# Performance work log

Measured on AMD Instinct MI355X. Metric: run time of the kernel, lower is better.

## Reference

```python
import jax, jax.numpy as jnp
import numpy as np
from jax import lax

B, C, H, W = 8, 512, 16, 16
Di, N, R, K = 1024, 16, 32, 4  # d_inner, d_state, dt_rank, num scan directions
EPS = 1e-5


def _ln(x, g, b):
    mu = x.mean(-1, keepdims=True)
    var = ((x - mu) ** 2).mean(-1, keepdims=True)
    return (x - mu) * lax.rsqrt(var + EPS) * g + b


def _ss2d_core(xc, x_proj_w, dt_w, dt_b, A_logs, Ds):
    # xc: (b, Di, H, W) after depthwise conv + SiLU. 4-direction selective scan.
    b = xc.shape[0]
    L = H * W
    x_flat = xc.reshape(b, Di, L)
    x_wh = xc.transpose(0, 1, 3, 2).reshape(b, Di, L)
    x_hwwh = jnp.stack([x_flat, x_wh], 1)                  # (b,2,Di,L)
    xs = jnp.concatenate([x_hwwh, x_hwwh[..., ::-1]], 1)   # (b,K,Di,L)
    x_dbl = jnp.einsum('bkdl,kcd->bkcl', xs, x_proj_w)     # (b,K,R+2N,L)
    dts, Bs, Cs = x_dbl[:, :, :R], x_dbl[:, :, R:R + N], x_dbl[:, :, R + N:]
    dts = jnp.einsum('bkrl,kdr->bkdl', dts, dt_w)
    delta = jax.nn.softplus(dts + dt_b[None, :, :, None])  # (b,K,Di,L)
    A = -jnp.exp(A_logs).reshape(K, Di, N)                 # (K,Di,N)

    def step(h, inp):
        d, u, Bl, Cl = inp  # d,u:(b,K,Di)  Bl,Cl:(b,K,N)
        h = jnp.exp(d[..., None] * A) * h + (d * u)[..., None] * Bl[:, :, None, :]
        yl = jnp.einsum('bkdn,bkn->bkd', h, Cl)
        return h, yl

    inps = (delta.transpose(3, 0, 1, 2), xs.transpose(3, 0, 1, 2),
            Bs.transpose(3, 0, 1, 2), Cs.transpose(3, 0, 1, 2))
    h0 = jnp.zeros((b, K, Di, N), xc.dtype)
    _, ys = lax.scan(step, h0, inps)                       # (L,b,K,Di)
    ys = ys.transpose(1, 2, 3, 0) + xs * Ds.reshape(1, K, Di, 1)  # + D*u skip
    inv = ys[:, 2:4, :, ::-1]
    wh = ys[:, 1].reshape(b, Di, W, H).transpose(0, 1, 3, 2).reshape(b, Di, L)
    invwh = inv[:, 1].reshape(b, Di, W, H).transpose(0, 1, 3, 2).reshape(b, Di, L)
    y = ys[:, 0] + inv[:, 0] + wh + invwh                  # (b,Di,L)
    return y.transpose(0, 2, 1).reshape(b, H, W, Di)


def _conv_ffn(x, ffn_conv_w, bn_g, bn_b, bn_mean, bn_var, fc1_w, fc2_w):
    x = lax.conv_general_dilated(x, ffn_conv_w, (1, 1), [(1, 1), (1, 1)],
                                 dimension_numbers=('NCHW', 'OIHW', 'NCHW'))
    x = ((x - bn_mean[:, None, None]) * lax.rsqrt(bn_var + EPS)[:, None, None]
         * bn_g[:, None, None] + bn_b[:, None, None])
    x = jnp.clip(x, 0.0, 6.0)                              # ReLU6
    x = jnp.einsum('bchw,oc->bohw', x, fc1_w)              # 1x1 conv fc1
    x = jax.nn.gelu(x, approximate=False)
    return jnp.einsum('bchw,oc->bohw', x, fc2_w)           # 1x1 conv fc2


def _forward(x, y, ln1_g, ln1_b, in_proj_w, conv_w, conv_b, x_proj_w, dt_w,
             dt_b, A_logs, Ds, out_norm_g, out_norm_b, out_proj_w, ffn_conv_w,
             bn_g, bn_b, bn_mean, bn_var, fc1_w, fc2_w, lin1_w, lin1_b,
             lin2_w, lin2_b):
    # --- VSSBlock: LN -> SS2D -> residual ---
    x1 = x.transpose(0, 2, 3, 1)                           # (B,H,W,C)
    xn = _ln(x1, ln1_g, ln1_b)
    xz = jnp.einsum('bhwc,oc->bhwo', xn, in_proj_w)        # in_proj (no bias)
    xa, z = xz[..., :Di], xz[..., Di:]
    xc = xa.transpose(0, 3, 1, 2)                          # (B,Di,H,W)
    xc = lax.conv_general_dilated(xc, conv_w, (1, 1), [(1, 1), (1, 1)],
                                  feature_group_count=Di,
                                  dimension_numbers=('NCHW', 'OIHW', 'NCHW'))
    xc = jax.nn.silu(xc + conv_b[:, None, None])
    yc = _ss2d_core(xc, x_proj_w, dt_w, dt_b, A_logs, Ds)  # (B,H,W,Di)
    yc = _ln(yc, out_norm_g, out_norm_b) * jax.nn.silu(z)
    vss = x1 + jnp.einsum('bhwd,od->bhwo', yc, out_proj_w)
    # --- ConvFFN ---
    xm = _conv_ffn(vss.transpose(0, 3, 1, 2), ffn_conv_w, bn_g, bn_b, bn_mean,
                   bn_var, fc1_w, fc2_w)                   # (B,C,H,W)
    # --- channel attention: both pools are AdaptiveAvgPool2d(1), so max==avg ---
    pooled = y.mean(axis=(2, 3))                           # (B,C)
    lin = jax.nn.relu(pooled @ lin1_w.T + lin1_b) @ lin2_w.T + lin2_b
    gate = jax.nn.sigmoid(2.0 * lin)                       # linear_max + linear_avg
    return gate[:, :, None, None] * xm


def setup_inputs() -> dict:
    key = jax.random.key(0)
    ks = jax.random.split(key, 16)
    n = lambda i, shape, s=0.05: jax.random.normal(ks[i], shape, jnp.float32) * s
    return {
        'x': n(0, (B, C, H, W), 1.0),
        'y': n(1, (B, C, H, W), 1.0),
        'ln1_g': jnp.ones((C,), jnp.float32), 'ln1_b': jnp.zeros((C,), jnp.float32),
        'in_proj_w': n(2, (2 * Di, C)),
        'conv_w': n(3, (Di, 1, 3, 3), 0.2), 'conv_b': jnp.zeros((Di,), jnp.float32),
        'x_proj_w': n(4, (K, R + 2 * N, Di)),
        'dt_w': n(5, (K, Di, R), 0.1), 'dt_b': n(6, (K, Di), 0.1),
        'A_logs': n(7, (K * Di, N), 0.1), 'Ds': jnp.ones((K * Di,), jnp.float32),
        'out_norm_g': jnp.ones((Di,), jnp.float32), 'out_norm_b': jnp.zeros((Di,), jnp.float32),
        'out_proj_w': n(8, (C, Di)),
        'ffn_conv_w': n(9, (C, C, 3, 3)),
        'bn_g': jnp.ones((C,), jnp.float32), 'bn_b': jnp.zeros((C,), jnp.float32),
        'bn_mean': jnp.zeros((C,), jnp.float32), 'bn_var': jnp.ones((C,), jnp.float32),
        'fc1_w': n(10, (C, C)), 'fc2_w': n(11, (C, C)),
        'lin1_w': n(12, (C // 2, C)), 'lin1_b': jnp.zeros((C // 2,), jnp.float32),
        'lin2_w': n(13, (C, C // 2)), 'lin2_b': jnp.zeros((C,), jnp.float32),
    }


def reference(x, y, ln1_g, ln1_b, in_proj_w, conv_w, conv_b, x_proj_w, dt_w,
              dt_b, A_logs, Ds, out_norm_g, out_norm_b, out_proj_w, ffn_conv_w,
              bn_g, bn_b, bn_mean, bn_var, fc1_w, fc2_w, lin1_w, lin1_b,
              lin2_w, lin2_b):
    return _forward(x, y, ln1_g, ln1_b, in_proj_w, conv_w, conv_b, x_proj_w,
                    dt_w, dt_b, A_logs, Ds, out_norm_g, out_norm_b, out_proj_w,
                    ffn_conv_w, bn_g, bn_b, bn_mean, bn_var, fc1_w, fc2_w,
                    lin1_w, lin1_b, lin2_w, lin2_b)
```

## Files before the change

kernel.cpp:

```cpp
#include <hip/hip_runtime.h>
#include <hip/hip_bf16.h>
#include <math.h>

#define DEV_INLINE __device__ __forceinline__

constexpr int B_ = 8, C_ = 512, L_ = 256;
constexpr float EPS_ = 1e-5f;

typedef __attribute__((ext_vector_type(8))) short bf16x8;
typedef __attribute__((ext_vector_type(4))) float f32x4;

DEV_INLINE int lmap1(int l) { return ((l & 15) << 4) | (l >> 4); }
DEV_INLINE float sigmoidf_(float x) { return 1.f / (1.f + __expf(-x)); }
DEV_INLINE float siluf_(float x) { return x * sigmoidf_(x); }
DEV_INLINE float ex2_(float x) { return __builtin_amdgcn_exp2f(x); }

DEV_INLINE unsigned pk2(float a, float b) {
    __hip_bfloat16 x = __float2bfloat16(a), y = __float2bfloat16(b);
    unsigned short ux = *reinterpret_cast<unsigned short*>(&x);
    unsigned short uy = *reinterpret_cast<unsigned short*>(&y);
    return ((unsigned)uy << 16) | ux;
}

__global__ __launch_bounds__(256) void k_pool(const float* __restrict__ y, float* __restrict__ pooled) {
    int bc = blockIdx.x;
    int t = threadIdx.x;
    __shared__ float red[256];
    red[t] = y[bc * 256 + t];
    __syncthreads();
    for (int s = 128; s > 0; s >>= 1) { if (t < s) red[t] += red[t + s]; __syncthreads(); }
    if (t == 0) pooled[bc] = red[0] * (1.f / 256.f);
}

__global__ __launch_bounds__(256) void k_gate(const float* __restrict__ pooled,
                                              const float* __restrict__ lin1_w, const float* __restrict__ lin1_b,
                                              const float* __restrict__ lin2_w, const float* __restrict__ lin2_b,
                                              float* __restrict__ gate) {
    int b = blockIdx.x;
    int t = threadIdx.x;
    __shared__ float p[512];
    __shared__ float h1[256];
    p[t] = pooled[b * 512 + t];
    p[t + 256] = pooled[b * 512 + t + 256];
    __syncthreads();
    float s = lin1_b[t];
    const float4* wp1 = (const float4*)(lin1_w + t * 512);
    #pragma unroll 4
    for (int c = 0; c < 128; ++c) {
        float4 pv = *(const float4*)(p + c * 4);
        float4 wv = wp1[c];
        s = fmaf(pv.x, wv.x, s); s = fmaf(pv.y, wv.y, s);
        s = fmaf(pv.z, wv.z, s); s = fmaf(pv.w, wv.w, s);
    }
    h1[t] = fmaxf(s, 0.f);
    __syncthreads();
    #pragma unroll
    for (int cc = 0; cc < 2; ++cc) {
        int c = t + cc * 256;
        float s2 = lin2_b[c];
        const float4* wp2 = (const float4*)(lin2_w + c * 256);
        #pragma unroll 4
        for (int j = 0; j < 64; ++j) {
            float4 hv = *(const float4*)(h1 + j * 4);
            float4 wv = wp2[j];
            s2 = fmaf(hv.x, wv.x, s2); s2 = fmaf(hv.y, wv.y, s2);
            s2 = fmaf(hv.z, wv.z, s2); s2 = fmaf(hv.w, wv.w, s2);
        }
        gate[b * 512 + c] = sigmoidf_(2.f * s2);
    }
}

__global__ __launch_bounds__(256) void k_ln(const float* __restrict__ x, const float* __restrict__ g,
                                            const float* __restrict__ bta, float* __restrict__ xn) {
    int pos = blockIdx.x;
    int b = pos >> 8, l = pos & 255;
    int t = threadIdx.x;
    float v0 = x[(b * C_ + t) * L_ + l];
    float v1 = x[(b * C_ + t + 256) * L_ + l];
    __shared__ float red[256];
    red[t] = v0 + v1;
    __syncthreads();
    for (int s = 128; s > 0; s >>= 1) { if (t < s) red[t] += red[t + s]; __syncthreads(); }
    float mu = red[0] * (1.f / 512.f);
    __syncthreads();
    float d0 = v0 - mu, d1 = v1 - mu;
    red[t] = d0 * d0 + d1 * d1;
    __syncthreads();
    for (int s = 128; s > 0; s >>= 1) { if (t < s) red[t] += red[t + s]; __syncthreads(); }
    float rs = rsqrtf(red[0] * (1.f / 512.f) + EPS_);
    xn[pos * C_ + t] = d0 * rs * g[t] + bta[t];
    xn[pos * C_ + t + 256] = d1 * rs * g[t + 256] + bta[t + 256];
}

__global__ __launch_bounds__(256) void k_wcast5(const float* __restrict__ ip, const float* __restrict__ xp,
                                                const float* __restrict__ op, const float* __restrict__ f1,
                                                const float* __restrict__ f2, const float* __restrict__ dtw,
                                                __hip_bfloat16* __restrict__ dst) {
    size_t e = ((size_t)blockIdx.x * 256 + threadIdx.x) * 4;
    const float* src; size_t off;
    if (e < 1048576) { src = ip; off = e; }
    else if (e < 1310720) { src = xp; off = e - 1048576; }
    else if (e < 1835008) { src = op; off = e - 1310720; }
    else if (e < 2097152) { src = f1; off = e - 1835008; }
    else if (e < 2359296) { src = f2; off = e - 2097152; }
    else { src = dtw; off = e - 2359296; }
    float4 v = *(const float4*)(src + off);
    uint2 o; o.x = pk2(v.x, v.y); o.y = pk2(v.z, v.w);
    *(uint2*)(dst + e) = o;
}

__global__ __launch_bounds__(256) void k_wcast(const float* __restrict__ w, __hip_bfloat16* __restrict__ wt) {
    int gid = blockIdx.x * 256 + threadIdx.x;
    const float* src = w + (size_t)gid * 9;
    #pragma unroll
    for (int tap = 0; tap < 9; ++tap) wt[(size_t)tap * 262144 + gid] = __float2bfloat16(src[tap]);
}

enum { M_INPROJ = 0, M_XDBL = 1, M_OUTPROJ = 2, M_FC1 = 3, M_FC2 = 4, M_DELTA = 5 };

template <int MODE>
__global__ __launch_bounds__(256) void gemm_mfma(const float* __restrict__ Af, const __hip_bfloat16* __restrict__ Wb,
                                                 float* __restrict__ O, float* __restrict__ O2,
                                                 const float* __restrict__ AUX, __hip_bfloat16* __restrict__ Ob) {
    constexpr int KK = (MODE == M_XDBL || MODE == M_OUTPROJ) ? 1024 : (MODE == M_DELTA) ? 32 : 512;
    __shared__ short Asm[64 * 32];
    __shared__ short Bsm[64 * 32];
    const int t = threadIdx.x;
    const int lane = t & 63, wv = t >> 6;
    int m0, n0 = 0, kdir = 0, bq = 0;
    if constexpr (MODE == M_XDBL) { m0 = blockIdx.x * 64; kdir = blockIdx.y; }
    else if constexpr (MODE == M_FC2) { bq = blockIdx.x >> 3; m0 = (blockIdx.x & 7) * 64; n0 = blockIdx.y * 64; }
    else { m0 = blockIdx.x * 64; n0 = blockIdx.y * 64; }
    const int kdel = (m0 >> 8) & 3;

    const int r_ = t >> 2, kq = t & 3;
    const int skey = (r_ >> 1) & 3;
    uint4* adst = (uint4*)(Asm + r_ * 32) + (kq ^ skey);
    uint4* bdst = (uint4*)(Bsm + r_ * 32) + (kq ^ skey);

    const float* arowf = nullptr;
    const __hip_bfloat16* arowb = nullptr;
    if constexpr (MODE == M_INPROJ) arowf = Af + (size_t)(m0 + r_) * 512 + kq * 8;
    else if constexpr (MODE == M_XDBL) {
        int m = m0 + r_; int b = m >> 8, l = m & 255;
        int lm = (kdir < 2) ? l : 255 - l;
        arowf = Af + (size_t)((b * 2 + (kdir & 1)) * 256 + lm) * 1024 + kq * 8;
    } else if constexpr (MODE == M_OUTPROJ) arowf = Af + (size_t)(m0 + r_) * 1024 + kq * 8;
    else if constexpr (MODE == M_FC1) arowf = Af + (size_t)(m0 + r_) * 512 + kq * 8;
    else if constexpr (MODE == M_DELTA) arowf = Af + (size_t)(m0 + r_) * 64 + kq * 8;
    else arowb = Wb + (size_t)(m0 + r_) * 512 + kq * 8;

    const __hip_bfloat16* browb = nullptr;
    const float* browf = nullptr;
    if constexpr (MODE == M_INPROJ) browb = Wb + (size_t)(n0 + r_) * 512 + kq * 8;
    else if constexpr (MODE == M_XDBL) browb = Wb + (size_t)(kdir * 64 + r_) * 1024 + kq * 8;
    else if constexpr (MODE == M_OUTPROJ) browb = Wb + (size_t)(n0 + r_) * 1024 + kq * 8;
    else if constexpr (MODE == M_FC1) browb = Wb + (size_t)(n0 + r_) * 512 + kq * 8;
    else if constexpr (MODE == M_DELTA) browb = Wb + ((size_t)(kdel * 1024 + n0 + r_)) * 32 + kq * 8;
    else browf = Af + (size_t)(bq * 256 + n0 + r_) * 512 + kq * 8;

    f32x4 acc[4];
    #pragma unroll
    for (int nf = 0; nf < 4; ++nf) acc[nf] = (f32x4){0.f, 0.f, 0.f, 0.f};

    for (int k0 = 0; k0 < KK; k0 += 32) {
        __syncthreads();
        if constexpr (MODE == M_FC2) {
            *adst = *(const uint4*)(arowb + k0);
            float4 u0 = *(const float4*)(browf + k0);
            float4 u1 = *(const float4*)(browf + k0 + 4);
            uint4 pk; pk.x = pk2(u0.x, u0.y); pk.y = pk2(u0.z, u0.w); pk.z = pk2(u1.x, u1.y); pk.w = pk2(u1.z, u1.w);
            *bdst = pk;
        } else {
            float4 u0 = *(const float4*)(arowf + k0);
            float4 u1 = *(const float4*)(arowf + k0 + 4);
            uint4 pk; pk.x = pk2(u0.x, u0.y); pk.y = pk2(u0.z, u0.w); pk.z = pk2(u1.x, u1.y); pk.w = pk2(u1.z, u1.w);
            *adst = pk;
            *bdst = *(const uint4*)(browb + k0);
        }
        __syncthreads();
        int mrow = wv * 16 + (lane & 15);
        int ks = lane >> 4;
        bf16x8 af = *(const bf16x8*)(Asm + mrow * 32 + ((ks ^ ((mrow >> 1) & 3)) * 8));
        #pragma unroll
        for (int nf = 0; nf < 4; ++nf) {
            int nrow = nf * 16 + (lane & 15);
            bf16x8 bfv = *(const bf16x8*)(Bsm + nrow * 32 + ((ks ^ ((nrow >> 1) & 3)) * 8));
            acc[nf] = __builtin_amdgcn_mfma_f32_16x16x32_bf16(af, bfv, acc[nf], 0, 0, 0);
        }
    }

    const int mlb = (lane >> 4) * 4, nl = lane & 15;
    #pragma unroll
    for (int nf = 0; nf < 4; ++nf) {
        #pragma unroll
        for (int j = 0; j < 4; ++j) {
            float v = acc[nf][j];
            int m_loc = wv * 16 + mlb + j;
            int n_loc = nf * 16 + nl;
            if constexpr (MODE == M_INPROJ) {
                int m = m0 + m_loc, n = n0 + n_loc;
                if (n0 < 1024) O[(size_t)m * 1024 + n] = v;
                else O2[(size_t)m * 1024 + (n - 1024)] = v;
            } else if constexpr (MODE == M_XDBL) {
                int m = m0 + m_loc; int b = m >> 8, l = m & 255;
                O[((size_t)(b * 4 + kdir) * 256 + l) * 64 + n_loc] = v;
            } else if constexpr (MODE == M_OUTPROJ) {
                int m = m0 + m_loc, n = n0 + n_loc; int b = m >> 8, l = m & 255;
                float f = AUX[((size_t)b * 512 + n) * 256 + l] + v;
                Ob[(size_t)m * 512 + n] = __float2bfloat16(f);
            } else if constexpr (MODE == M_FC1) {
                int m = m0 + m_loc, n = n0 + n_loc;
                O[(size_t)m * 512 + n] = 0.5f * v * (1.f + erff(v * 0.70710678118f));
            } else if constexpr (MODE == M_DELTA) {
                int m = m0 + m_loc, n = n0 + n_loc;
                int bkk = m >> 8, l = m & 255;
                float v2 = v + AUX[kdel * 1024 + n];
                float dlt = (v2 > 20.f) ? v2 : __logf(1.f + __expf(v2));
                O[((((size_t)bkk * 32) + (n >> 5)) * 256 + l) * 32 + (n & 31)] = dlt;
            } else {
                int c = m0 + m_loc, n = n0 + n_loc;
                O[((size_t)(bq * 512 + c)) * 256 + n] = v * AUX[bq * 512 + c];
            }
        }
    }
}

__global__ __launch_bounds__(256) void k_dwconv2(const float* __restrict__ xa, const float* __restrict__ cw,
                                                 const float* __restrict__ cb, float* __restrict__ xs_t) {
    int pos = blockIdx.x;
    int b = pos >> 8, l = pos & 255;
    int h = l >> 4, w = l & 15;
    int t = threadIdx.x;
    int d = t * 4;
    float wv[36];
    {
        const float4* cp = (const float4*)(cw + (size_t)d * 9);
        #pragma unroll
        for (int j = 0; j < 9; ++j) { float4 v = cp[j]; wv[j*4] = v.x; wv[j*4+1] = v.y; wv[j*4+2] = v.z; wv[j*4+3] = v.w; }
    }
    float4 bias = *(const float4*)(cb + d);
    float a0 = bias.x, a1 = bias.y, a2 = bias.z, a3 = bias.w;
    #pragma unroll
    for (int ky = -1; ky <= 1; ++ky) {
        int hh = h + ky;
        if ((unsigned)hh >= 16u) continue;
        #pragma unroll
        for (int kx = -1; kx <= 1; ++kx) {
            int ww = w + kx;
            if ((unsigned)ww >= 16u) continue;
            float4 v = *(const float4*)(xa + (size_t)(b * 256 + hh * 16 + ww) * 1024 + d);
            int tap = (ky + 1) * 3 + (kx + 1);
            a0 = fmaf(v.x, wv[0 * 9 + tap], a0);
            a1 = fmaf(v.y, wv[1 * 9 + tap], a1);
            a2 = fmaf(v.z, wv[2 * 9 + tap], a2);
            a3 = fmaf(v.w, wv[3 * 9 + tap], a3);
        }
    }
    float4 o; o.x = siluf_(a0); o.y = siluf_(a1); o.z = siluf_(a2); o.w = siluf_(a3);
    *(float4*)(xs_t + ((size_t)(b * 2 + 0) * 256 + l) * 1024 + d) = o;
    *(float4*)(xs_t + ((size_t)(b * 2 + 1) * 256 + lmap1(l)) * 1024 + d) = o;
}

__global__ __launch_bounds__(512) void k_scan7(const float* __restrict__ xs_t, const float* __restrict__ x_dbl,
                                               const float* __restrict__ A_logs, const float* __restrict__ Ds,
                                               float* __restrict__ dys) {
    const int bk = blockIdx.x >> 5;
    const int db = blockIdx.x & 31;
    const int b = bk >> 2, k = bk & 3;
    const int t = threadIdx.x;
    const int c = t >> 5, dd = t & 31;
    const int d = db * 32 + dd;
    const bool rev = (k >= 2);

    __shared__ float Ssh[16][33];
    __shared__ float locH[16][32][17];

    float An2[16];
    {
        const float* alp = A_logs + (size_t)(k * 1024 + d) * 16;
        #pragma unroll
        for (int i = 0; i < 16; ++i) An2[i] = -__expf(alp[i]) * 1.44269504088896f;
    }
    const float Dv = Ds[k * 1024 + d];

    const int lbeg = c * 16;
    float* yp = dys + (((size_t)bk * 32 + db) * 256 + lbeg) * 32 + dd;
    const float* up = xs_t + ((size_t)(b * 2 + (k & 1)) * 256 + (rev ? 255 - lbeg : lbeg)) * 1024 + d;
    const ptrdiff_t ustr = rev ? -1024 : 1024;
    const float* xc = x_dbl + (size_t)bk * 256 * 64 + lbeg * 64;

    float h[16];
    #pragma unroll
    for (int i = 0; i < 16; ++i) h[i] = 0.f;
    float S = 0.f;

    #pragma unroll 4
    for (int li = 0; li < 16; ++li) {
        float dl = yp[li * 32];
        float u = up[(ptrdiff_t)li * ustr];
        S += dl;
        float du = dl * u;
        #pragma unroll
        for (int q = 0; q < 4; ++q) {
            float4 Bq = *(const float4*)(xc + li * 64 + 32 + q * 4);
            h[q*4+0] = fmaf(ex2_(dl * An2[q*4+0]), h[q*4+0], du * Bq.x);
            h[q*4+1] = fmaf(ex2_(dl * An2[q*4+1]), h[q*4+1], du * Bq.y);
            h[q*4+2] = fmaf(ex2_(dl * An2[q*4+2]), h[q*4+2], du * Bq.z);
            h[q*4+3] = fmaf(ex2_(dl * An2[q*4+3]), h[q*4+3], du * Bq.w);
        }
    }
    Ssh[c][dd] = S;
    #pragma unroll
    for (int i = 0; i < 16; ++i) locH[c][dd][i] = h[i];
    __syncthreads();

    #pragma unroll
    for (int i = 0; i < 16; ++i) h[i] = 0.f;
    for (int j = 0; j < c; ++j) {
        float Sj = Ssh[j][dd];
        #pragma unroll
        for (int i = 0; i < 16; ++i) h[i] = fmaf(ex2_(Sj * An2[i]), h[i], locH[j][dd][i]);
    }

    #pragma unroll 4
    for (int li = 0; li < 16; ++li) {
        float dl = yp[li * 32];
        float u = up[(ptrdiff_t)li * ustr];
        float du = dl * u;
        float yv = 0.f;
        #pragma unroll
        for (int q = 0; q < 4; ++q) {
            float4 Bq = *(const float4*)(xc + li * 64 + 32 + q * 4);
            float4 Cq = *(const float4*)(xc + li * 64 + 48 + q * 4);
            h[q*4+0] = fmaf(ex2_(dl * An2[q*4+0]), h[q*4+0], du * Bq.x); yv = fmaf(h[q*4+0], Cq.x, yv);
            h[q*4+1] = fmaf(ex2_(dl * An2[q*4+1]), h[q*4+1], du * Bq.y); yv = fmaf(h[q*4+1], Cq.y, yv);
            h[q*4+2] = fmaf(ex2_(dl * An2[q*4+2]), h[q*4+2], du * Bq.z); yv = fmaf(h[q*4+2], Cq.z, yv);
            h[q*4+3] = fmaf(ex2_(dl * An2[q*4+3]), h[q*4+3], du * Bq.w); yv = fmaf(h[q*4+3], Cq.w, yv);
        }
        yp[li * 32] = yv + u * Dv;
    }
}

__global__ __launch_bounds__(256) void k_combine(const float* __restrict__ dys, const float* __restrict__ z,
                                                 const float* __restrict__ g, const float* __restrict__ bb,
                                                 float* __restrict__ yc) {
    int pos = blockIdx.x;
    int b = pos >> 8, l = pos & 255;
    int t = threadIdx.x;
    int lw = lmap1(l);
    int db0 = t >> 5, dd = t & 31;
    float v[4];
    float psum = 0.f;
    #pragma unroll
    for (int q = 0; q < 4; ++q) {
        int dbq = db0 + q * 8;
        float s0 = dys[((((size_t)(b * 4 + 0) * 32) + dbq) * 256 + l) * 32 + dd];
        float s1 = dys[((((size_t)(b * 4 + 1) * 32) + dbq) * 256 + lw) * 32 + dd];
        float s2 = dys[((((size_t)(b * 4 + 2) * 32) + dbq) * 256 + (255 - l)) * 32 + dd];
        float s3 = dys[((((size_t)(b * 4 + 3) * 32) + dbq) * 256 + (255 - lw)) * 32 + dd];
        v[q] = s0 + s1 + s2 + s3;
        psum += v[q];
    }
    __shared__ float red[256];
    red[t] = psum;
    __syncthreads();
    for (int s = 128; s > 0; s >>= 1) { if (t < s) red[t] += red[t + s]; __syncthreads(); }
    float mu = red[0] * (1.f / 1024.f);
    __syncthreads();
    float p2 = 0.f;
    #pragma unroll
    for (int q = 0; q < 4; ++q) { float ddv = v[q] - mu; p2 += ddv * ddv; }
    red[t] = p2;
    __syncthreads();
    for (int s = 128; s > 0; s >>= 1) { if (t < s) red[t] += red[t + s]; __syncthreads(); }
    float rs = rsqrtf(red[0] * (1.f / 1024.f) + EPS_);
    #pragma unroll
    for (int q = 0; q < 4; ++q) {
        int d = (db0 + q * 8) * 32 + dd;
        float zn = z[(size_t)pos * 1024 + d];
        yc[(size_t)pos * 1024 + d] = ((v[q] - mu) * rs * g[d] + bb[d]) * siluf_(zn);
    }
}

__global__ __launch_bounds__(256) void k_conv2m(const __hip_bfloat16* __restrict__ vssb,
                                                const __hip_bfloat16* __restrict__ wt,
                                                float* __restrict__ convp) {
    __shared__ short Asm[18 * 18 * 32];
    __shared__ short Bsm[9 * 64 * 32];
    const int b = blockIdx.x, co0 = blockIdx.y * 64, split = blockIdx.z;
    const int t = threadIdx.x;
    const int lane = t & 63, wid = t >> 6;
    const int wcol = lane & 15, slot = lane >> 4;

    f32x4 acc[4][4];
    #pragma unroll
    for (int r = 0; r < 4; ++r)
        #pragma unroll
        for (int g = 0; g < 4; ++g) acc[r][g] = (f32x4){0.f, 0.f, 0.f, 0.f};

    for (int ch = 0; ch < 2; ++ch) {
        const int ci0 = split * 64 + ch * 32;
        __syncthreads();
        for (int i = t; i < 324; i += 256) {
            int row = i / 18, col = i - row * 18;
            uint4 v0 = {0,0,0,0}, v1 = {0,0,0,0}, v2 = {0,0,0,0}, v3 = {0,0,0,0};
            if (row >= 1 && row <= 16 && col >= 1 && col <= 16) {
                const uint4* src = (const uint4*)(vssb + ((size_t)(b * 256 + (row - 1) * 16 + (col - 1)) * 512 + ci0));
                v0 = src[0]; v1 = src[1]; v2 = src[2]; v3 = src[3];
            }
            uint4* dst = (uint4*)(Asm + i * 32);
            int key = (col >> 1) & 3;
            dst[0 ^ key] = v0; dst[1 ^ key] = v1; dst[2 ^ key] = v2; dst[3 ^ key] = v3;
        }
        for (int i = t; i < 576; i += 256) {
            int tap = i >> 6, col = i & 63;
            const uint4* src = (const uint4*)(wt + ((size_t)(tap * 512 + co0 + col) * 512 + ci0));
            uint4* dst = (uint4*)(Bsm + i * 32);
            int key = (col >> 1) & 3;
            dst[0 ^ key] = src[0]; dst[1 ^ key] = src[1]; dst[2 ^ key] = src[2]; dst[3 ^ key] = src[3];
        }
        __syncthreads();
        #pragma unroll
        for (int tap = 0; tap < 9; ++tap) {
            const int ky = tap / 3, kx = tap - ky * 3;
            bf16x8 af[4], bfr[4];
            #pragma unroll
            for (int r = 0; r < 4; ++r) {
                int crow = wid * 4 + r + ky;
                int ccol = wcol + kx;
                int s2 = slot ^ ((ccol >> 1) & 3);
                af[r] = *(const bf16x8*)(Asm + ((crow * 18 + ccol) * 32 + s2 * 8));
            }
            #pragma unroll
            for (int g = 0; g < 4; ++g) {
                int col = g * 16 + wcol;
                int s2 = slot ^ ((col >> 1) & 3);
                bfr[g] = *(const bf16x8*)(Bsm + ((tap * 64 + col) * 32 + s2 * 8));
            }
            #pragma unroll
            for (int r = 0; r < 4; ++r)
                #pragma unroll
                for (int g = 0; g < 4; ++g)
                    acc[r][g] = __builtin_amdgcn_mfma_f32_16x16x32_bf16(af[r], bfr[g], acc[r][g], 0, 0, 0);
        }
    }
    float* base = convp + (size_t)split * 1048576 + (size_t)b * 512 * 256;
    #pragma unroll
    for (int r = 0; r < 4; ++r) {
        int h = wid * 4 + r;
        #pragma unroll
        for (int g = 0; g < 4; ++g) {
            int co = co0 + g * 16 + wcol;
            *(f32x4*)(base + (size_t)co * 256 + h * 16 + slot * 4) = acc[r][g];
        }
    }
}

__global__ __launch_bounds__(256) void k_convred2(const float* __restrict__ convp,
                                                  const float* __restrict__ bn_g, const float* __restrict__ bn_b,
                                                  const float* __restrict__ bn_mean, const float* __restrict__ bn_var,
                                                  float* __restrict__ t1) {
    int b = blockIdx.x >> 7, cb = (blockIdx.x >> 3) & 15, pb = blockIdx.x & 7;
    int co0 = cb * 32, pos0 = pb * 32;
    int t = threadIdx.x;
    int ti = t >> 5, tj = t & 31;
    __shared__ float tile[32][33];
    #pragma unroll
    for (int r = 0; r < 4; ++r) {
        int co = co0 + ti + r * 8;
        size_t idx = ((size_t)b * 512 + co) * 256 + pos0 + tj;
        float s = 0.f;
        #pragma unroll
        for (int sp = 0; sp < 8; ++sp) s += convp[idx + (size_t)sp * 1048576];
        float o = (s - bn_mean[co]) * rsqrtf(bn_var[co] + EPS_) * bn_g[co] + bn_b[co];
        tile[ti + r * 8][tj] = fminf(fmaxf(o, 0.f), 6.f);
    }
    __syncthreads();
    #pragma unroll
    for (int r = 0; r < 4; ++r) {
        int pos = pos0 + ti + r * 8;
        t1[((size_t)b * 256 + pos) * 512 + co0 + tj] = tile[tj][ti + r * 8];
    }
}

extern "C" void kernel_launch(void* const* d_in, const int* in_sizes, int n_in,
                              void* d_out, int out_size, void* d_ws, size_t ws_size,
                              hipStream_t stream) {
    const float* x = (const float*)d_in[0];
    const float* y = (const float*)d_in[1];
    const float* ln1_g = (const float*)d_in[2];
    const float* ln1_b = (const float*)d_in[3];
    const float* in_proj_w = (const float*)d_in[4];
    const float* conv_w = (const float*)d_in[5];
    const float* conv_b = (const float*)d_in[6];
    const float* x_proj_w = (const float*)d_in[7];
    const float* dt_w = (const float*)d_in[8];
    const float* dt_b = (const float*)d_in[9];
    const float* A_logs = (const float*)d_in[10];
    const float* Ds = (const float*)d_in[11];
    const float* out_norm_g = (const float*)d_in[12];
    const float* out_norm_b = (const float*)d_in[13];
    const float* out_proj_w = (const float*)d_in[14];
    const float* ffn_conv_w = (const float*)d_in[15];
    const float* bn_g = (const float*)d_in[16];
    const float* bn_b = (const float*)d_in[17];
    const float* bn_mean = (const float*)d_in[18];
    const float* bn_var = (const float*)d_in[19];
    const float* fc1_w = (const float*)d_in[20];
    const float* fc2_w = (const float*)d_in[21];
    const float* lin1_w = (const float*)d_in[22];
    const float* lin1_b = (const float*)d_in[23];
    const float* lin2_w = (const float*)d_in[24];
    const float* lin2_b = (const float*)d_in[25];
    float* out = (float*)d_out;

    char* ws = (char*)d_ws;
    size_t off = 0;
    auto alloc = [&](size_t nf) { float* p = (float*)(ws + off); off += nf * sizeof(float); return p; };
    float* xn    = alloc(2048u * 512);
    float* xa    = alloc(2048u * 1024);
    float* z     = alloc(2048u * 1024);
    float* xs_t  = alloc(2u * 2048 * 1024);
    float* x_dbl = alloc(8u * 4 * 256 * 64);
    float* ys_t  = alloc(4u * 2048 * 1024);
    float* wb    = alloc(1245184);
    float* pooled = alloc(4096);
    float* gate   = alloc(4096);

    float* yc = xa;
    float* t1 = xs_t;
    float* t2 = xs_t + 2048u * 512;
    __hip_bfloat16* vssb = (__hip_bfloat16*)xn;
    __hip_bfloat16* w_t  = (__hip_bfloat16*)z;
    float* convp = ys_t;
    __hip_bfloat16* inprojb = (__hip_bfloat16*)wb;
    __hip_bfloat16* xprojb  = inprojb + 1048576;
    __hip_bfloat16* outprojb = xprojb + 262144;
    __hip_bfloat16* fc1b = outprojb + 524288;
    __hip_bfloat16* fc2b = fc1b + 262144;
    __hip_bfloat16* dtwb = fc2b + 262144;

    k_wcast5<<<2432, 256, 0, stream>>>(in_proj_w, x_proj_w, out_proj_w, fc1_w, fc2_w, dt_w, inprojb);
    k_pool<<<4096, 256, 0, stream>>>(y, pooled);
    k_gate<<<8, 256, 0, stream>>>(pooled, lin1_w, lin1_b, lin2_w, lin2_b, gate);
    k_ln<<<2048, 256, 0, stream>>>(x, ln1_g, ln1_b, xn);
    gemm_mfma<M_INPROJ><<<dim3(32, 32), 256, 0, stream>>>(xn, inprojb, xa, z, nullptr, nullptr);
    k_dwconv2<<<2048, 256, 0, stream>>>(xa, conv_w, conv_b, xs_t);
    gemm_mfma<M_XDBL><<<dim3(32, 4), 256, 0, stream>>>(xs_t, xprojb, x_dbl, nullptr, nullptr, nullptr);
    gemm_mfma<M_DELTA><<<dim3(128, 16), 256, 0, stream>>>(x_dbl, dtwb, ys_t, nullptr, dt_b, nullptr);
    k_scan7<<<1024, 512, 0, stream>>>(xs_t, x_dbl, A_logs, Ds, ys_t);
    k_combine<<<2048, 256, 0, stream>>>(ys_t, z, out_norm_g, out_norm_b, yc);
    k_wcast<<<1024, 256, 0, stream>>>(ffn_conv_w, w_t);
    gemm_mfma<M_OUTPROJ><<<dim3(32, 8), 256, 0, stream>>>(yc, outprojb, nullptr, nullptr, x, vssb);
    k_conv2m<<<dim3(8, 8, 8), 256, 0, stream>>>(vssb, w_t, convp);
    k_convred2<<<1024, 256, 0, stream>>>(convp, bn_g, bn_b, bn_mean, bn_var, t1);
    gemm_mfma<M_FC1><<<dim3(32, 8), 256, 0, stream>>>(t1, fc1b, t2, nullptr, nullptr, nullptr);
    gemm_mfma<M_FC2><<<dim3(64, 4), 256, 0, stream>>>(t2, fc2b, out, nullptr, gate, nullptr);
}
```

Baseline: 259.7 us.

## Emit bf16 activations from producer kernels and merge conv weight cast

Producer kernels (layernorm, combine, conv reduction, FC1 GELU epilogue) now write bf16 instead of fp32. The consuming GEMMs can then copy A tiles straight into shared memory without converting, which halves activation traffic and drops the per-tile packing. The separate conv-weight cast kernel is merged into the batch weight-cast launch, removing one launch. The scan kernel also keeps delta and u in registers from its first pass instead of reloading them in the second, at the cost of more register pressure.

```diff
diff --git a/kernel.cpp b/kernel.cpp
--- a/kernel.cpp
+++ b/kernel.cpp
@@ -71,7 +71,7 @@
 }
 
 __global__ __launch_bounds__(256) void k_ln(const float* __restrict__ x, const float* __restrict__ g,
-                                            const float* __restrict__ bta, float* __restrict__ xn) {
+                                            const float* __restrict__ bta, __hip_bfloat16* __restrict__ xnb) {
     int pos = blockIdx.x;
     int b = pos >> 8, l = pos & 255;
     int t = threadIdx.x;
@@ -88,41 +88,43 @@
     __syncthreads();
     for (int s = 128; s > 0; s >>= 1) { if (t < s) red[t] += red[t + s]; __syncthreads(); }
     float rs = rsqrtf(red[0] * (1.f / 512.f) + EPS_);
-    xn[pos * C_ + t] = d0 * rs * g[t] + bta[t];
-    xn[pos * C_ + t + 256] = d1 * rs * g[t + 256] + bta[t + 256];
-}
-
-__global__ __launch_bounds__(256) void k_wcast5(const float* __restrict__ ip, const float* __restrict__ xp,
+    xnb[pos * C_ + t] = __float2bfloat16(d0 * rs * g[t] + bta[t]);
+    xnb[pos * C_ + t + 256] = __float2bfloat16(d1 * rs * g[t + 256] + bta[t + 256]);
+}
+
+__global__ __launch_bounds__(256) void k_wcast6(const float* __restrict__ ip, const float* __restrict__ xp,
                                                 const float* __restrict__ op, const float* __restrict__ f1,
                                                 const float* __restrict__ f2, const float* __restrict__ dtw,
-                                                __hip_bfloat16* __restrict__ dst) {
-    size_t e = ((size_t)blockIdx.x * 256 + threadIdx.x) * 4;
-    const float* src; size_t off;
-    if (e < 1048576) { src = ip; off = e; }
-    else if (e < 1310720) { src = xp; off = e - 1048576; }
-    else if (e < 1835008) { src = op; off = e - 1310720; }
-    else if (e < 2097152) { src = f1; off = e - 1835008; }
-    else if (e < 2359296) { src = f2; off = e - 2097152; }
-    else { src = dtw; off = e - 2359296; }
-    float4 v = *(const float4*)(src + off);
-    uint2 o; o.x = pk2(v.x, v.y); o.y = pk2(v.z, v.w);
-    *(uint2*)(dst + e) = o;
-}
-
-__global__ __launch_bounds__(256) void k_wcast(const float* __restrict__ w, __hip_bfloat16* __restrict__ wt) {
-    int gid = blockIdx.x * 256 + threadIdx.x;
-    const float* src = w + (size_t)gid * 9;
-    #pragma unroll
-    for (int tap = 0; tap < 9; ++tap) wt[(size_t)tap * 262144 + gid] = __float2bfloat16(src[tap]);
+                                                const float* __restrict__ fw, __hip_bfloat16* __restrict__ dst) {
+    if (blockIdx.x < 2432) {
+        size_t e = ((size_t)blockIdx.x * 256 + threadIdx.x) * 4;
+        const float* src; size_t off;
+        if (e < 1048576) { src = ip; off = e; }
+        else if (e < 1310720) { src = xp; off = e - 1048576; }
+        else if (e < 1835008) { src = op; off = e - 1310720; }
+        else if (e < 2097152) { src = f1; off = e - 1835008; }
+        else if (e < 2359296) { src = f2; off = e - 2097152; }
+        else { src = dtw; off = e - 2359296; }
+        float4 v = *(const float4*)(src + off);
+        uint2 o; o.x = pk2(v.x, v.y); o.y = pk2(v.z, v.w);
+        *(uint2*)(dst + e) = o;
+    } else {
+        int gid = (blockIdx.x - 2432) * 256 + threadIdx.x;
+        __hip_bfloat16* wt = dst + 2490368;
+        const float* src = fw + (size_t)gid * 9;
+        #pragma unroll
+        for (int tap = 0; tap < 9; ++tap) wt[(size_t)tap * 262144 + gid] = __float2bfloat16(src[tap]);
+    }
 }
 
 enum { M_INPROJ = 0, M_XDBL = 1, M_OUTPROJ = 2, M_FC1 = 3, M_FC2 = 4, M_DELTA = 5 };
 
 template <int MODE>
-__global__ __launch_bounds__(256) void gemm_mfma(const float* __restrict__ Af, const __hip_bfloat16* __restrict__ Wb,
+__global__ __launch_bounds__(256) void gemm_mfma(const void* __restrict__ Aptr, const __hip_bfloat16* __restrict__ Wb,
                                                  float* __restrict__ O, float* __restrict__ O2,
                                                  const float* __restrict__ AUX, __hip_bfloat16* __restrict__ Ob) {
     constexpr int KK = (MODE == M_XDBL || MODE == M_OUTPROJ) ? 1024 : (MODE == M_DELTA) ? 32 : 512;
+    constexpr bool A_COPY = (MODE == M_INPROJ || MODE == M_OUTPROJ || MODE == M_FC1 || MODE == M_FC2);
     __shared__ short Asm[64 * 32];
     __shared__ short Bsm[64 * 32];
     const int t = threadIdx.x;
@@ -140,24 +142,23 @@
 
     const float* arowf = nullptr;
     const __hip_bfloat16* arowb = nullptr;
-    if constexpr (MODE == M_INPROJ) arowf = Af + (size_t)(m0 + r_) * 512 + kq * 8;
+    if constexpr (MODE == M_INPROJ) arowb = (const __hip_bfloat16*)Aptr + (size_t)(m0 + r_) * 512 + kq * 8;
     else if constexpr (MODE == M_XDBL) {
         int m = m0 + r_; int b = m >> 8, l = m & 255;
         int lm = (kdir < 2) ? l : 255 - l;
-        arowf = Af + (size_t)((b * 2 + (kdir & 1)) * 256 + lm) * 1024 + kq * 8;
-    } else if constexpr (MODE == M_OUTPROJ) arowf = Af + (size_t)(m0 + r_) * 1024 + kq * 8;
-    else if constexpr (MODE == M_FC1) arowf = Af + (size_t)(m0 + r_) * 512 + kq * 8;
-    else if constexpr (MODE == M_DELTA) arowf = Af + (size_t)(m0 + r_) * 64 + kq * 8;
+        arowf = (const float*)Aptr + (size_t)((b * 2 + (kdir & 1)) * 256 + lm) * 1024 + kq * 8;
+    } else if constexpr (MODE == M_OUTPROJ) arowb = (const __hip_bfloat16*)Aptr + (size_t)(m0 + r_) * 1024 + kq * 8;
+    else if constexpr (MODE == M_FC1) arowb = (const __hip_bfloat16*)Aptr + (size_t)(m0 + r_) * 512 + kq * 8;
+    else if constexpr (MODE == M_DELTA) arowf = (const float*)Aptr + (size_t)(m0 + r_) * 64 + kq * 8;
     else arowb = Wb + (size_t)(m0 + r_) * 512 + kq * 8;
 
     const __hip_bfloat16* browb = nullptr;
-    const float* browf = nullptr;
     if constexpr (MODE == M_INPROJ) browb = Wb + (size_t)(n0 + r_) * 512 + kq * 8;
     else if constexpr (MODE == M_XDBL) browb = Wb + (size_t)(kdir * 64 + r_) * 1024 + kq * 8;
     else if constexpr (MODE == M_OUTPROJ) browb = Wb + (size_t)(n0 + r_) * 1024 + kq * 8;
     else if constexpr (MODE == M_FC1) browb = Wb + (size_t)(n0 + r_) * 512 + kq * 8;
     else if constexpr (MODE == M_DELTA) browb = Wb + ((size_t)(kdel * 1024 + n0 + r_)) * 32 + kq * 8;
-    else browf = Af + (size_t)(bq * 256 + n0 + r_) * 512 + kq * 8;
+    else browb = (const __hip_bfloat16*)Aptr + (size_t)(bq * 256 + n0 + r_) * 512 + kq * 8;
 
     f32x4 acc[4];
     #pragma unroll
@@ -165,19 +166,15 @@
 
     for (int k0 = 0; k0 < KK; k0 += 32) {
         __syncthreads();
-        if constexpr (MODE == M_FC2) {
+        if constexpr (A_COPY) {
             *adst = *(const uint4*)(arowb + k0);
-            float4 u0 = *(const float4*)(browf + k0);
-            float4 u1 = *(const float4*)(browf + k0 + 4);
-            uint4 pk; pk.x = pk2(u0.x, u0.y); pk.y = pk2(u0.z, u0.w); pk.z = pk2(u1.x, u1.y); pk.w = pk2(u1.z, u1.w);
-            *bdst = pk;
         } else {
             float4 u0 = *(const float4*)(arowf + k0);
             float4 u1 = *(const float4*)(arowf + k0 + 4);
             uint4 pk; pk.x = pk2(u0.x, u0.y); pk.y = pk2(u0.z, u0.w); pk.z = pk2(u1.x, u1.y); pk.w = pk2(u1.z, u1.w);
             *adst = pk;
-            *bdst = *(const uint4*)(browb + k0);
-        }
+        }
+        *bdst = *(const uint4*)(browb + k0);
         __syncthreads();
         int mrow = wv * 16 + (lane & 15);
         int ks = lane >> 4;
@@ -211,7 +208,8 @@
                 Ob[(size_t)m * 512 + n] = __float2bfloat16(f);
             } else if constexpr (MODE == M_FC1) {
                 int m = m0 + m_loc, n = n0 + n_loc;
-                O[(size_t)m * 512 + n] = 0.5f * v * (1.f + erff(v * 0.70710678118f));
+                float gl = 0.5f * v * (1.f + erff(v * 0.70710678118f));
+                Ob[(size_t)m * 512 + n] = __float2bfloat16(gl);
             } else if constexpr (MODE == M_DELTA) {
                 int m = m0 + m_loc, n = n0 + n_loc;
                 int bkk = m >> 8, l = m & 255;
@@ -262,7 +260,7 @@
     *(float4*)(xs_t + ((size_t)(b * 2 + 1) * 256 + lmap1(l)) * 1024 + d) = o;
 }
 
-__global__ __launch_bounds__(512) void k_scan7(const float* __restrict__ xs_t, const float* __restrict__ x_dbl,
+__global__ __launch_bounds__(512) void k_scan8(const float* __restrict__ xs_t, const float* __restrict__ x_dbl,
                                                const float* __restrict__ A_logs, const float* __restrict__ Ds,
                                                float* __restrict__ dys) {
     const int bk = blockIdx.x >> 5;
@@ -294,11 +292,13 @@
     #pragma unroll
     for (int i = 0; i < 16; ++i) h[i] = 0.f;
     float S = 0.f;
-
-    #pragma unroll 4
+    float dls[16], us_[16];
+
+    #pragma unroll
     for (int li = 0; li < 16; ++li) {
         float dl = yp[li * 32];
         float u = up[(ptrdiff_t)li * ustr];
+        dls[li] = dl; us_[li] = u;
         S += dl;
         float du = dl * u;
         #pragma unroll
@@ -323,10 +323,10 @@
         for (int i = 0; i < 16; ++i) h[i] = fmaf(ex2_(Sj * An2[i]), h[i], locH[j][dd][i]);
     }
 
-    #pragma unroll 4
+    #pragma unroll
     for (int li = 0; li < 16; ++li) {
-        float dl = yp[li * 32];
-        float u = up[(ptrdiff_t)li * ustr];
+        float dl = dls[li];
+        float u = us_[li];
         float du = dl * u;
         float yv = 0.f;
         #pragma unroll
@@ -344,7 +344,7 @@
 
 __global__ __launch_bounds__(256) void k_combine(const float* __restrict__ dys, const float* __restrict__ z,
                                                  const float* __restrict__ g, const float* __restrict__ bb,
-                                                 float* __restrict__ yc) {
+                                                 __hip_bfloat16* __restrict__ ycb) {
     int pos = blockIdx.x;
     int b = pos >> 8, l = pos & 255;
     int t = threadIdx.x;
@@ -379,7 +379,8 @@
     for (int q = 0; q < 4; ++q) {
         int d = (db0 + q * 8) * 32 + dd;
         float zn = z[(size_t)pos * 1024 + d];
-        yc[(size_t)pos * 1024 + d] = ((v[q] - mu) * rs * g[d] + bb[d]) * siluf_(zn);
+        float o = ((v[q] - mu) * rs * g[d] + bb[d]) * siluf_(zn);
+        ycb[(size_t)pos * 1024 + d] = __float2bfloat16(o);
     }
 }
 
@@ -460,7 +461,7 @@
 __global__ __launch_bounds__(256) void k_convred2(const float* __restrict__ convp,
                                                   const float* __restrict__ bn_g, const float* __restrict__ bn_b,
                                                   const float* __restrict__ bn_mean, const float* __restrict__ bn_var,
-                                                  float* __restrict__ t1) {
+                                                  __hip_bfloat16* __restrict__ t1b) {
     int b = blockIdx.x >> 7, cb = (blockIdx.x >> 3) & 15, pb = blockIdx.x & 7;
     int co0 = cb * 32, pos0 = pb * 32;
     int t = threadIdx.x;
@@ -480,7 +481,7 @@
     #pragma unroll
     for (int r = 0; r < 4; ++r) {
         int pos = pos0 + ti + r * 8;
-        t1[((size_t)b * 256 + pos) * 512 + co0 + tj] = tile[tj][ti + r * 8];
+        t1b[((size_t)b * 256 + pos) * 512 + co0 + tj] = __float2bfloat16(tile[tj][ti + r * 8]);
     }
 }
 
@@ -524,15 +525,15 @@
     float* xs_t  = alloc(2u * 2048 * 1024);
     float* x_dbl = alloc(8u * 4 * 256 * 64);
     float* ys_t  = alloc(4u * 2048 * 1024);
-    float* wb    = alloc(1245184);
+    float* wb    = alloc(2424832);
     float* pooled = alloc(4096);
     float* gate   = alloc(4096);
 
-    float* yc = xa;
-    float* t1 = xs_t;
-    float* t2 = xs_t + 2048u * 512;
+    __hip_bfloat16* xnb = (__hip_bfloat16*)xn;
     __hip_bfloat16* vssb = (__hip_bfloat16*)xn;
-    __hip_bfloat16* w_t  = (__hip_bfloat16*)z;
+    __hip_bfloat16* ycb = (__hip_bfloat16*)xa;
+    __hip_bfloat16* t1b = (__hip_bfloat16*)xs_t;
+    __hip_bfloat16* t2b = (__hip_bfloat16*)(xs_t + 2048u * 512);
     float* convp = ys_t;
     __hip_bfloat16* inprojb = (__hip_bfloat16*)wb;
     __hip_bfloat16* xprojb  = inprojb + 1048576;
@@ -540,21 +541,21 @@
     __hip_bfloat16* fc1b = outprojb + 524288;
     __hip_bfloat16* fc2b = fc1b + 262144;
     __hip_bfloat16* dtwb = fc2b + 262144;
-
-    k_wcast5<<<2432, 256, 0, stream>>>(in_proj_w, x_proj_w, out_proj_w, fc1_w, fc2_w, dt_w, inprojb);
+    __hip_bfloat16* w_t  = dtwb + 131072;
+
+    k_wcast6<<<3456, 256, 0, stream>>>(in_proj_w, x_proj_w, out_proj_w, fc1_w, fc2_w, dt_w, ffn_conv_w, inprojb);
     k_pool<<<4096, 256, 0, stream>>>(y, pooled);
     k_gate<<<8, 256, 0, stream>>>(pooled, lin1_w, lin1_b, lin2_w, lin2_b, gate);
-    k_ln<<<2048, 256, 0, stream>>>(x, ln1_g, ln1_b, xn);
-    gemm_mfma<M_INPROJ><<<dim3(32, 32), 256, 0, stream>>>(xn, inprojb, xa, z, nullptr, nullptr);
+    k_ln<<<2048, 256, 0, stream>>>(x, ln1_g, ln1_b, xnb);
+    gemm_mfma<M_INPROJ><<<dim3(32, 32), 256, 0, stream>>>(xnb, inprojb, xa, z, nullptr, nullptr);
     k_dwconv2<<<2048, 256, 0, stream>>>(xa, conv_w, conv_b, xs_t);
     gemm_mfma<M_XDBL><<<dim3(32, 4), 256, 0, stream>>>(xs_t, xprojb, x_dbl, nullptr, nullptr, nullptr);
     gemm_mfma<M_DELTA><<<dim3(128, 16), 256, 0, stream>>>(x_dbl, dtwb, ys_t, nullptr, dt_b, nullptr);
-    k_scan7<<<1024, 512, 0, stream>>>(xs_t, x_dbl, A_logs, Ds, ys_t);
-    k_combine<<<2048, 256, 0, stream>>>(ys_t, z, out_norm_g, out_norm_b, yc);
-    k_wcast<<<1024, 256, 0, stream>>>(ffn_conv_w, w_t);
-    gemm_mfma<M_OUTPROJ><<<dim3(32, 8), 256, 0, stream>>>(yc, outprojb, nullptr, nullptr, x, vssb);
+    k_scan8<<<1024, 512, 0, stream>>>(xs_t, x_dbl, A_logs, Ds, ys_t);
+    k_combine<<<2048, 256, 0, stream>>>(ys_t, z, out_norm_g, out_norm_b, ycb);
+    gemm_mfma<M_OUTPROJ><<<dim3(32, 8), 256, 0, stream>>>(ycb, outprojb, nullptr, nullptr, x, vssb);
     k_conv2m<<<dim3(8, 8, 8), 256, 0, stream>>>(vssb, w_t, convp);
-    k_convred2<<<1024, 256, 0, stream>>>(convp, bn_g, bn_b, bn_mean, bn_var, t1);
-    gemm_mfma<M_FC1><<<dim3(32, 8), 256, 0, stream>>>(t1, fc1b, t2, nullptr, nullptr, nullptr);
-    gemm_mfma<M_FC2><<<dim3(64, 4), 256, 0, stream>>>(t2, fc2b, out, nullptr, gate, nullptr);
-}
+    k_convred2<<<1024, 256, 0, stream>>>(convp, bn_g, bn_b, bn_mean, bn_var, t1b);
+    gemm_mfma<M_FC1><<<dim3(32, 8), 256, 0, stream>>>(t1b, fc1b, nullptr, nullptr, nullptr, t2b);
+    gemm_mfma<M_FC2><<<dim3(64, 4), 256, 0, stream>>>(t2b, fc2b, out, nullptr, gate, nullptr);
+}
```

Measured after the change: 327.2 us. 26.0% more time.
